# Performance work log

Measured on AMD Instinct MI355X. Metric: run time of the kernel, lower is better.

## Reference

```python
import jax, jax.numpy as jnp
import numpy as np

ALPHA = 0.025
BETA = 0.00025
V_TH = 1.0
EXP_TAU = 50.0          # tau_v / dt
T_NOW = 10.0            # current simulation step counter self.t
REFRAC_STEPS = 2        # refractory_period / dt
INV_TAU_V = float(np.exp(-1.0 / 50.0))   # exp(-dt/tau_v)
INV_TAU_I = float(np.exp(-1.0))          # exp(-dt/tau_i)
INV_TAU_V_PAIR = INV_TAU_V               # tau_v_pair defaults to tau_v
INV_TAU_I_PAIR = INV_TAU_I               # tau_i_pair defaults to tau_i

B, N = 32, 4096


def setup_inputs() -> dict:
    key = jax.random.key(0)
    ks = jax.random.split(key, 8)
    return {
        "inp": jax.random.normal(ks[0], (B, N), jnp.float32),
        "W_rec": jax.random.uniform(ks[1], (N, N), jnp.float32),  # nonneg dense adjacency weights
        "mem_pot": jax.random.normal(ks[2], (B, N), jnp.float32),
        "mem_cur": jax.random.normal(ks[3], (B, N), jnp.float32),
        "mem_pot_paired": jax.random.normal(ks[4], (B, N), jnp.float32),
        "mem_cur_paired": jax.random.normal(ks[5], (B, N), jnp.float32),
        "st": jnp.zeros((N,), jnp.float32),
        "refrac_neurons": jax.random.randint(ks[6], (B, N), 0, 3, jnp.int32),
    }


def reference(inp, W_rec, mem_pot, mem_cur, mem_pot_paired, mem_cur_paired, st, refrac_neurons):
    sign_mask = W_rec > 0  # torch: sign(W_rec) > 0 (weights are nonneg)

    # decrement refractory counters
    refrac = jnp.where(refrac_neurons > 0, refrac_neurons - 1, refrac_neurons)

    # threshold (ceil+clamp -> {0,1} spikes)
    S = jnp.clip(jnp.ceil(mem_pot - V_TH), 0.0, 1.0)                     # (B,N)
    S_paired = jnp.clip(jnp.ceil(mem_pot_paired - V_TH - ALPHA), 0.0, 1.0)

    # ---- plasticity weight update ----
    sp_max = S_paired.max(axis=0)            # (N,)
    st_new = jnp.where(S > 0, T_NOW, st)     # broadcasts (N,) -> (B,N), as in torch
    max_st = st_new.max(axis=0)              # (N,)
    # meshgrid(a,b) with ij indexing: |a-b|[i,j] = |max_st[i]-max_st[j]|
    diff = jnp.abs(max_st[:, None] - max_st[None, :])                    # (N,N)
    update_mask = (sp_max[:, None] > 0) & sign_mask                      # (N,N)
    updated = W_rec + BETA - jnp.where(update_mask,
                                       ALPHA * jnp.exp(diff / EXP_TAU),
                                       0.0)
    updated = jnp.clip(updated, 0.0, 1.0)
    W_new = jnp.where(sign_mask, updated, W_rec)

    # ---- integrate ----
    active = refrac == 0
    mem_cur_n = jnp.where(active, inp + S @ W_new + mem_cur, mem_cur)
    mem_cur_p_n = jnp.where(active, S @ W_new.T + mem_cur_paired, mem_cur_paired)
    mem_pot_n = jnp.where(active, mem_cur_n + mem_pot, mem_pot)
    mem_pot_p_n = jnp.where(active, mem_cur_p_n + mem_pot_paired, mem_pot_paired)

    # leak
    mem_pot_n = mem_pot_n * INV_TAU_V
    mem_cur_n = mem_cur_n * INV_TAU_I
    mem_pot_p_n = mem_pot_p_n * INV_TAU_V_PAIR
    mem_cur_p_n = mem_cur_p_n * INV_TAU_I_PAIR

    # reset spiked neurons
    mem_pot_n = jnp.where(S > 0, 0.0, mem_pot_n)
    mem_pot_p_n = jnp.where(S_paired > 0, 0.0, mem_pot_p_n)
    refrac_new = jnp.where(S > 0, REFRAC_STEPS, refrac)

    return S, mem_pot_n, W_new, mem_cur_n, mem_pot_p_n, mem_cur_p_n, refrac_new
```

## Files before the change

kernel.cpp:

```cpp
#include <hip/hip_runtime.h>
#include <cstdint>
#include <cstddef>

constexpr int N = 4096;
constexpr int B = 32;
constexpr int BN = B * N;
constexpr size_t NN = (size_t)N * N;
constexpr int KCHUNKS = 4;
constexpr int KC = N / KCHUNKS;

constexpr float ALPHA = 0.025f;
constexpr float BETA = 0.00025f;
constexpr float T_NOW = 10.0f;
constexpr float INV_EXP_TAU = 0.02f;
constexpr float INV_TAU_V = 0.98019867f;
constexpr float INV_TAU_I = 0.36787944f;

typedef __attribute__((ext_vector_type(8))) short short8;
typedef __attribute__((ext_vector_type(4))) float f32x4;

__device__ inline unsigned short f2bf(float f) {
  uint32_t u = __float_as_uint(f);
  u += 0x7FFFu + ((u >> 16) & 1u);
  return (unsigned short)(u >> 16);
}

__global__ __launch_bounds__(256) void pass_a(
    const float* __restrict__ mem_pot, const float* __restrict__ mem_pot_p,
    const float* __restrict__ st, float* __restrict__ S_out,
    unsigned short* __restrict__ S_bf,
    uint32_t* __restrict__ maskS, uint32_t* __restrict__ maskSP,
    float* __restrict__ max_st, float* __restrict__ rowfac) {
  int j = blockIdx.x * blockDim.x + threadIdx.x;
  if (j >= N) return;
  float stj = st[j];
  uint32_t ms = 0u, msp = 0u;
  float maxv = -3.0e38f;
  #pragma unroll
  for (int b = 0; b < B; ++b) {
    float p = mem_pot[b * N + j];
    float pp = mem_pot_p[b * N + j];
    bool s = (p - 1.0f) > 0.0f;
    bool sp = ((pp - 1.0f) - ALPHA) > 0.0f;
    S_out[b * N + j] = s ? 1.0f : 0.0f;
    S_bf[b * N + j] = s ? 0x3F80u : 0u;
    ms |= (uint32_t)s << b;
    msp |= (uint32_t)sp << b;
    maxv = fmaxf(maxv, s ? T_NOW : stj);
  }
  maskS[j] = ms;
  maskSP[j] = msp;
  max_st[j] = maxv;
  rowfac[j] = msp ? ALPHA : 0.0f;
}

__global__ __launch_bounds__(256) void pass_b(
    const float* __restrict__ W, const float* __restrict__ max_st,
    const float* __restrict__ rowfac, float* __restrict__ Wout) {
  int i = blockIdx.x;
  int tid = threadIdx.x;
  float mst_i = max_st[i];
  float fac_i = rowfac[i];

  const float4* __restrict__ Wrow = (const float4*)(W + (size_t)i * N);
  float4* __restrict__ Wo = (float4*)(Wout + (size_t)i * N);
  const float4* __restrict__ mstv = (const float4*)max_st;

  float4 w[4], mj[4];
  #pragma unroll
  for (int it = 0; it < 4; ++it) {
    int idx = it * 256 + tid;
    w[it] = Wrow[idx];
    mj[it] = mstv[idx];
  }

  auto upd = [&](float ww, float mstj) -> float {
    float d = fabsf(mst_i - mstj);
    float ex = __expf(d * INV_EXP_TAU);
    float u = ww + BETA - fac_i * ex;
    u = fminf(fmaxf(u, 0.0f), 1.0f);
    return (ww > 0.0f) ? u : ww;
  };

  #pragma unroll
  for (int it = 0; it < 4; ++it) {
    int idx = it * 256 + tid;
    float4 wo;
    wo.x = upd(w[it].x, mj[it].x);
    wo.y = upd(w[it].y, mj[it].y);
    wo.z = upd(w[it].z, mj[it].z);
    wo.w = upd(w[it].w, mj[it].w);
    Wo[idx] = wo;
  }
}

__global__ __launch_bounds__(256) void pass_mfma(
    const float* __restrict__ Wn, const unsigned short* __restrict__ S_bf,
    float* __restrict__ partSW, float* __restrict__ partSWT) {
  int wv = threadIdx.x >> 6;
  int lane = threadIdx.x & 63;
  int ntile = blockIdx.x * 4 + wv;
  int j0 = ntile * 16;
  int kchunk = blockIdx.y;
  int kbase = kchunk * KC;
  int gemm = blockIdx.z;
  int quad = lane >> 4;
  int nl = lane & 15;

  f32x4 acc0 = {0.f, 0.f, 0.f, 0.f};
  f32x4 acc1 = {0.f, 0.f, 0.f, 0.f};
  const unsigned short* A0p = S_bf + (size_t)nl * N;
  const unsigned short* A1p = S_bf + (size_t)(nl + 16) * N;

  if (gemm == 0) {
    #pragma unroll 4
    for (int it = 0; it < KC / 32; ++it) {
      int k0 = kbase + it * 32;
      short8 a0 = *(const short8*)(A0p + k0 + quad * 8);
      short8 a1 = *(const short8*)(A1p + k0 + quad * 8);
      short8 bf;
      #pragma unroll
      for (int i = 0; i < 8; ++i) {
        float f = Wn[(size_t)(k0 + quad * 8 + i) * N + j0 + nl];
        bf[i] = (short)f2bf(f);
      }
      acc0 = __builtin_amdgcn_mfma_f32_16x16x32_bf16(a0, bf, acc0, 0, 0, 0);
      acc1 = __builtin_amdgcn_mfma_f32_16x16x32_bf16(a1, bf, acc1, 0, 0, 0);
    }
  } else {
    const float4* __restrict__ Wr =
        (const float4*)(Wn + (size_t)(j0 + nl) * N);
    #pragma unroll 4
    for (int it = 0; it < KC / 32; ++it) {
      int k0 = kbase + it * 32;
      short8 a0 = *(const short8*)(A0p + k0 + quad * 8);
      short8 a1 = *(const short8*)(A1p + k0 + quad * 8);
      int f4 = (k0 + quad * 8) >> 2;
      float4 f0 = Wr[f4];
      float4 f1 = Wr[f4 + 1];
      short8 bf;
      bf[0] = (short)f2bf(f0.x); bf[1] = (short)f2bf(f0.y);
      bf[2] = (short)f2bf(f0.z); bf[3] = (short)f2bf(f0.w);
      bf[4] = (short)f2bf(f1.x); bf[5] = (short)f2bf(f1.y);
      bf[6] = (short)f2bf(f1.z); bf[7] = (short)f2bf(f1.w);
      acc0 = __builtin_amdgcn_mfma_f32_16x16x32_bf16(a0, bf, acc0, 0, 0, 0);
      acc1 = __builtin_amdgcn_mfma_f32_16x16x32_bf16(a1, bf, acc1, 0, 0, 0);
    }
  }

  float* part = (gemm == 0) ? partSW : partSWT;
  size_t base = (size_t)kchunk * BN + j0 + nl;
  #pragma unroll
  for (int r = 0; r < 4; ++r) {
    part[base + (size_t)(quad * 4 + r) * N] = acc0[r];
    part[base + (size_t)(16 + quad * 4 + r) * N] = acc1[r];
  }
}

__global__ __launch_bounds__(256) void pass_d(
    const float* __restrict__ inp, const float* __restrict__ mem_pot,
    const float* __restrict__ mem_cur, const float* __restrict__ mem_pot_p,
    const float* __restrict__ mem_cur_p, const int* __restrict__ refrac_in,
    const uint32_t* __restrict__ maskS, const uint32_t* __restrict__ maskSP,
    const float* __restrict__ partSW, const float* __restrict__ partSWT,
    float* __restrict__ pot_out, float* __restrict__ cur_out,
    float* __restrict__ potp_out, float* __restrict__ curp_out,
    float* __restrict__ refrac_out) {
  int e = blockIdx.x * 256 + threadIdx.x;
  int b = e >> 12;
  int j = e & (N - 1);

  float SW = 0.0f, SWT = 0.0f;
  #pragma unroll
  for (int c = 0; c < KCHUNKS; ++c) {
    SW += partSW[(size_t)c * BN + e];
    SWT += partSWT[(size_t)c * BN + e];
  }

  int r = refrac_in[e];
  int rd = (r > 0) ? (r - 1) : r;
  bool active = (rd == 0);
  bool s = (maskS[j] >> b) & 1u;
  bool sp = (maskSP[j] >> b) & 1u;
  float cur = mem_cur[e], pot = mem_pot[e];
  float curp = mem_cur_p[e], potp = mem_pot_p[e];

  float cur_n = active ? (inp[e] + SW + cur) : cur;
  float curp_n = active ? (SWT + curp) : curp;
  float pot_n = active ? (cur_n + pot) : pot;
  float potp_n = active ? (curp_n + potp) : potp;

  pot_n *= INV_TAU_V;
  cur_n *= INV_TAU_I;
  potp_n *= INV_TAU_V;
  curp_n *= INV_TAU_I;

  if (s) pot_n = 0.0f;
  if (sp) potp_n = 0.0f;
  int rn = s ? 2 : rd;

  pot_out[e] = pot_n;
  cur_out[e] = cur_n;
  potp_out[e] = potp_n;
  curp_out[e] = curp_n;
  refrac_out[e] = (float)rn;
}

extern "C" void kernel_launch(void* const* d_in, const int* in_sizes, int n_in,
                              void* d_out, int out_size, void* d_ws, size_t ws_size,
                              hipStream_t stream) {
  const float* inp = (const float*)d_in[0];
  const float* W = (const float*)d_in[1];
  const float* mem_pot = (const float*)d_in[2];
  const float* mem_cur = (const float*)d_in[3];
  const float* mem_pot_p = (const float*)d_in[4];
  const float* mem_cur_p = (const float*)d_in[5];
  const float* st = (const float*)d_in[6];
  const int* refrac = (const int*)d_in[7];

  float* out = (float*)d_out;
  float* S_out = out;
  float* pot_out = out + BN;
  float* W_out = out + 2 * (size_t)BN;
  float* cur_out = W_out + NN;
  float* potp_out = cur_out + BN;
  float* curp_out = potp_out + BN;
  float* refrac_out = curp_out + BN;

  uint32_t* maskS = (uint32_t*)d_ws;
  uint32_t* maskSP = maskS + N;
  float* max_st = (float*)(maskSP + N);
  float* rowfac = max_st + N;
  unsigned short* S_bf = (unsigned short*)(rowfac + N);
  float* partSW = (float*)(S_bf + BN);
  float* partSWT = partSW + (size_t)KCHUNKS * BN;

  pass_a<<<N / 256, 256, 0, stream>>>(mem_pot, mem_pot_p, st, S_out, S_bf,
                                      maskS, maskSP, max_st, rowfac);
  pass_b<<<N, 256, 0, stream>>>(W, max_st, rowfac, W_out);
  pass_mfma<<<dim3(64, KCHUNKS, 2), 256, 0, stream>>>(W_out, S_bf, partSW,
                                                      partSWT);
  pass_d<<<BN / 256, 256, 0, stream>>>(inp, mem_pot, mem_cur, mem_pot_p,
                                       mem_cur_p, refrac, maskS, maskSP,
                                       partSW, partSWT, pot_out, cur_out,
                                       potp_out, curp_out, refrac_out);
}
```

Baseline: 167.1 us.

## Fuse weight update into MFMA GEMMs and reduce partials with atomics

Drops the separate weight-update pass. Both GEMM branches now read the original W and apply the plasticity update on the fly. The transposed-GEMM branch also writes the updated W out, so W_new is produced inside the GEMM. This removes one full N×N read and write of the updated matrix. Split-K partial buffers are replaced by float atomicAdd into a single zeroed accumulator (zeroed in pass_a), and KCHUNKS rises to 8. The cost is duplicated exp work in the non-transposed branch and atomic contention, and summation order becomes nondeterministic.

New measurement: 171.2 us. 1.02x slower.

```diff
diff --git a/kernel.cpp b/kernel.cpp
--- a/kernel.cpp
+++ b/kernel.cpp
@@ -6,7 +6,7 @@
 constexpr int B = 32;
 constexpr int BN = B * N;
 constexpr size_t NN = (size_t)N * N;
-constexpr int KCHUNKS = 4;
+constexpr int KCHUNKS = 8;
 constexpr int KC = N / KCHUNKS;
 
 constexpr float ALPHA = 0.025f;
@@ -25,14 +25,27 @@
   return (unsigned short)(u >> 16);
 }
 
+__device__ inline float wupd(float w, float mrow, float frow, float mcol) {
+  float d = fabsf(mrow - mcol);
+  float u = w + BETA - frow * __expf(d * INV_EXP_TAU);
+  u = fminf(fmaxf(u, 0.0f), 1.0f);
+  return (w > 0.0f) ? u : w;
+}
+
 __global__ __launch_bounds__(256) void pass_a(
     const float* __restrict__ mem_pot, const float* __restrict__ mem_pot_p,
     const float* __restrict__ st, float* __restrict__ S_out,
     unsigned short* __restrict__ S_bf,
     uint32_t* __restrict__ maskS, uint32_t* __restrict__ maskSP,
-    float* __restrict__ max_st, float* __restrict__ rowfac) {
+    float* __restrict__ max_st, float* __restrict__ rowfac,
+    float4* __restrict__ zero_region ) {
   int j = blockIdx.x * blockDim.x + threadIdx.x;
   if (j >= N) return;
+
+  float4 z = {0.0f, 0.0f, 0.0f, 0.0f};
+  #pragma unroll
+  for (int k = 0; k < 16; ++k) zero_region[j + k * 4096] = z;
+
   float stj = st[j];
   uint32_t ms = 0u, msp = 0u;
   float maxv = -3.0e38f;
@@ -54,58 +67,28 @@
   rowfac[j] = msp ? ALPHA : 0.0f;
 }
 
-__global__ __launch_bounds__(256) void pass_b(
-    const float* __restrict__ W, const float* __restrict__ max_st,
-    const float* __restrict__ rowfac, float* __restrict__ Wout) {
-  int i = blockIdx.x;
+__global__ __launch_bounds__(256) void pass_fused(
+    const float* __restrict__ W, const unsigned short* __restrict__ S_bf,
+    const float* __restrict__ max_st, const float* __restrict__ rowfac,
+    float* __restrict__ Wout, float* __restrict__ SW, float* __restrict__ SWT) {
+  __shared__ float mstK[KC];
+  __shared__ float facK[KC];
+
   int tid = threadIdx.x;
-  float mst_i = max_st[i];
-  float fac_i = rowfac[i];
-
-  const float4* __restrict__ Wrow = (const float4*)(W + (size_t)i * N);
-  float4* __restrict__ Wo = (float4*)(Wout + (size_t)i * N);
-  const float4* __restrict__ mstv = (const float4*)max_st;
-
-  float4 w[4], mj[4];
-  #pragma unroll
-  for (int it = 0; it < 4; ++it) {
-    int idx = it * 256 + tid;
-    w[it] = Wrow[idx];
-    mj[it] = mstv[idx];
-  }
-
-  auto upd = [&](float ww, float mstj) -> float {
-    float d = fabsf(mst_i - mstj);
-    float ex = __expf(d * INV_EXP_TAU);
-    float u = ww + BETA - fac_i * ex;
-    u = fminf(fmaxf(u, 0.0f), 1.0f);
-    return (ww > 0.0f) ? u : ww;
-  };
-
-  #pragma unroll
-  for (int it = 0; it < 4; ++it) {
-    int idx = it * 256 + tid;
-    float4 wo;
-    wo.x = upd(w[it].x, mj[it].x);
-    wo.y = upd(w[it].y, mj[it].y);
-    wo.z = upd(w[it].z, mj[it].z);
-    wo.w = upd(w[it].w, mj[it].w);
-    Wo[idx] = wo;
-  }
-}
-
-__global__ __launch_bounds__(256) void pass_mfma(
-    const float* __restrict__ Wn, const unsigned short* __restrict__ S_bf,
-    float* __restrict__ partSW, float* __restrict__ partSWT) {
-  int wv = threadIdx.x >> 6;
-  int lane = threadIdx.x & 63;
+  int wv = tid >> 6;
+  int lane = tid & 63;
   int ntile = blockIdx.x * 4 + wv;
   int j0 = ntile * 16;
-  int kchunk = blockIdx.y;
-  int kbase = kchunk * KC;
+  int kbase = blockIdx.y * KC;
   int gemm = blockIdx.z;
   int quad = lane >> 4;
   int nl = lane & 15;
+
+  for (int t = tid; t < KC; t += 256) {
+    mstK[t] = max_st[kbase + t];
+    facK[t] = rowfac[kbase + t];
+  }
+  __syncthreads();
 
   f32x4 acc0 = {0.f, 0.f, 0.f, 0.f};
   f32x4 acc1 = {0.f, 0.f, 0.f, 0.f};
@@ -113,47 +96,74 @@
   const unsigned short* A1p = S_bf + (size_t)(nl + 16) * N;
 
   if (gemm == 0) {
-    #pragma unroll 4
+    float mj = max_st[j0 + nl];
+    #pragma unroll 2
     for (int it = 0; it < KC / 32; ++it) {
-      int k0 = kbase + it * 32;
-      short8 a0 = *(const short8*)(A0p + k0 + quad * 8);
-      short8 a1 = *(const short8*)(A1p + k0 + quad * 8);
+      int ko = it * 32 + quad * 8;
+      int kg = kbase + ko;
+      short8 a0 = *(const short8*)(A0p + kg);
+      short8 a1 = *(const short8*)(A1p + kg);
+      const float* wp = W + (size_t)kg * N + j0 + nl;
+      float4 m4a = *(const float4*)(mstK + ko);
+      float4 m4b = *(const float4*)(mstK + ko + 4);
+      float4 f4a = *(const float4*)(facK + ko);
+      float4 f4b = *(const float4*)(facK + ko + 4);
+      float w[8];
+      #pragma unroll
+      for (int i = 0; i < 8; ++i) w[i] = wp[(size_t)i * N];
       short8 bf;
-      #pragma unroll
-      for (int i = 0; i < 8; ++i) {
-        float f = Wn[(size_t)(k0 + quad * 8 + i) * N + j0 + nl];
-        bf[i] = (short)f2bf(f);
-      }
+      bf[0] = (short)f2bf(wupd(w[0], m4a.x, f4a.x, mj));
+      bf[1] = (short)f2bf(wupd(w[1], m4a.y, f4a.y, mj));
+      bf[2] = (short)f2bf(wupd(w[2], m4a.z, f4a.z, mj));
+      bf[3] = (short)f2bf(wupd(w[3], m4a.w, f4a.w, mj));
+      bf[4] = (short)f2bf(wupd(w[4], m4b.x, f4b.x, mj));
+      bf[5] = (short)f2bf(wupd(w[5], m4b.y, f4b.y, mj));
+      bf[6] = (short)f2bf(wupd(w[6], m4b.z, f4b.z, mj));
+      bf[7] = (short)f2bf(wupd(w[7], m4b.w, f4b.w, mj));
       acc0 = __builtin_amdgcn_mfma_f32_16x16x32_bf16(a0, bf, acc0, 0, 0, 0);
       acc1 = __builtin_amdgcn_mfma_f32_16x16x32_bf16(a1, bf, acc1, 0, 0, 0);
     }
   } else {
-    const float4* __restrict__ Wr =
-        (const float4*)(Wn + (size_t)(j0 + nl) * N);
-    #pragma unroll 4
+    float mi = max_st[j0 + nl];
+    float fi = rowfac[j0 + nl];
+    const float* __restrict__ Wr = W + (size_t)(j0 + nl) * N;
+    float* __restrict__ Wor = Wout + (size_t)(j0 + nl) * N;
+    #pragma unroll 2
     for (int it = 0; it < KC / 32; ++it) {
-      int k0 = kbase + it * 32;
-      short8 a0 = *(const short8*)(A0p + k0 + quad * 8);
-      short8 a1 = *(const short8*)(A1p + k0 + quad * 8);
-      int f4 = (k0 + quad * 8) >> 2;
-      float4 f0 = Wr[f4];
-      float4 f1 = Wr[f4 + 1];
+      int ko = it * 32 + quad * 8;
+      int kg = kbase + ko;
+      short8 a0 = *(const short8*)(A0p + kg);
+      short8 a1 = *(const short8*)(A1p + kg);
+      float4 f0 = *(const float4*)(Wr + kg);
+      float4 f1 = *(const float4*)(Wr + kg + 4);
+      float4 m4a = *(const float4*)(mstK + ko);
+      float4 m4b = *(const float4*)(mstK + ko + 4);
+      float4 u0, u1;
+      u0.x = wupd(f0.x, mi, fi, m4a.x);
+      u0.y = wupd(f0.y, mi, fi, m4a.y);
+      u0.z = wupd(f0.z, mi, fi, m4a.z);
+      u0.w = wupd(f0.w, mi, fi, m4a.w);
+      u1.x = wupd(f1.x, mi, fi, m4b.x);
+      u1.y = wupd(f1.y, mi, fi, m4b.y);
+      u1.z = wupd(f1.z, mi, fi, m4b.z);
+      u1.w = wupd(f1.w, mi, fi, m4b.w);
+      *(float4*)(Wor + kg) = u0;
+      *(float4*)(Wor + kg + 4) = u1;
       short8 bf;
-      bf[0] = (short)f2bf(f0.x); bf[1] = (short)f2bf(f0.y);
-      bf[2] = (short)f2bf(f0.z); bf[3] = (short)f2bf(f0.w);
-      bf[4] = (short)f2bf(f1.x); bf[5] = (short)f2bf(f1.y);
-      bf[6] = (short)f2bf(f1.z); bf[7] = (short)f2bf(f1.w);
+      bf[0] = (short)f2bf(u0.x); bf[1] = (short)f2bf(u0.y);
+      bf[2] = (short)f2bf(u0.z); bf[3] = (short)f2bf(u0.w);
+      bf[4] = (short)f2bf(u1.x); bf[5] = (short)f2bf(u1.y);
+      bf[6] = (short)f2bf(u1.z); bf[7] = (short)f2bf(u1.w);
       acc0 = __builtin_amdgcn_mfma_f32_16x16x32_bf16(a0, bf, acc0, 0, 0, 0);
       acc1 = __builtin_amdgcn_mfma_f32_16x16x32_bf16(a1, bf, acc1, 0, 0, 0);
     }
   }
 
-  float* part = (gemm == 0) ? partSW : partSWT;
-  size_t base = (size_t)kchunk * BN + j0 + nl;
+  float* dst = (gemm == 0) ? SW : SWT;
   #pragma unroll
   for (int r = 0; r < 4; ++r) {
-    part[base + (size_t)(quad * 4 + r) * N] = acc0[r];
-    part[base + (size_t)(16 + quad * 4 + r) * N] = acc1[r];
+    atomicAdd(dst + (size_t)(quad * 4 + r) * N + j0 + nl, acc0[r]);
+    atomicAdd(dst + (size_t)(16 + quad * 4 + r) * N + j0 + nl, acc1[r]);
   }
 }
 
@@ -162,7 +172,7 @@
     const float* __restrict__ mem_cur, const float* __restrict__ mem_pot_p,
     const float* __restrict__ mem_cur_p, const int* __restrict__ refrac_in,
     const uint32_t* __restrict__ maskS, const uint32_t* __restrict__ maskSP,
-    const float* __restrict__ partSW, const float* __restrict__ partSWT,
+    const float* __restrict__ SWbuf, const float* __restrict__ SWTbuf,
     float* __restrict__ pot_out, float* __restrict__ cur_out,
     float* __restrict__ potp_out, float* __restrict__ curp_out,
     float* __restrict__ refrac_out) {
@@ -170,12 +180,8 @@
   int b = e >> 12;
   int j = e & (N - 1);
 
-  float SW = 0.0f, SWT = 0.0f;
-  #pragma unroll
-  for (int c = 0; c < KCHUNKS; ++c) {
-    SW += partSW[(size_t)c * BN + e];
-    SWT += partSWT[(size_t)c * BN + e];
-  }
+  float SW = SWbuf[e];
+  float SWT = SWTbuf[e];
 
   int r = refrac_in[e];
   int rd = (r > 0) ? (r - 1) : r;
@@ -232,16 +238,16 @@
   float* max_st = (float*)(maskSP + N);
   float* rowfac = max_st + N;
   unsigned short* S_bf = (unsigned short*)(rowfac + N);
-  float* partSW = (float*)(S_bf + BN);
-  float* partSWT = partSW + (size_t)KCHUNKS * BN;
+  float* SW = (float*)(S_bf + BN);
+  float* SWT = SW + BN;
 
   pass_a<<<N / 256, 256, 0, stream>>>(mem_pot, mem_pot_p, st, S_out, S_bf,
-                                      maskS, maskSP, max_st, rowfac);
-  pass_b<<<N, 256, 0, stream>>>(W, max_st, rowfac, W_out);
-  pass_mfma<<<dim3(64, KCHUNKS, 2), 256, 0, stream>>>(W_out, S_bf, partSW,
-                                                      partSWT);
+                                      maskS, maskSP, max_st, rowfac,
+                                      (float4*)SW);
+  pass_fused<<<dim3(64, KCHUNKS, 2), 256, 0, stream>>>(W, S_bf, max_st, rowfac,
+                                                       W_out, SW, SWT);
   pass_d<<<BN / 256, 256, 0, stream>>>(inp, mem_pot, mem_cur, mem_pot_p,
                                        mem_cur_p, refrac, maskS, maskSP,
-                                       partSW, partSWT, pot_out, cur_out,
+                                       SW, SWT, pot_out, cur_out,
                                        potp_out, curp_out, refrac_out);
 }
```

## Fuse weight update with both S@W and S@W^T MFMA GEMMs via LDS tiles

Applied to the files above, without the earlier changes.

Merges the elementwise plasticity update and the two bf16 MFMA matmuls into one tiled kernel. Each block updates a 256x128 tile of W, writes W_out, and stages bf16 copies in LDS so that half the waves compute S@W and the other half compute S@W^T from the same tile. This avoids re-reading the 64MB updated W from global memory twice. The cost is many more partial-sum buffers (16 and 32 slices) for the final pass to reduce, plus extra workspace traffic.

Measured after the change: 156.0 us. -6.6%, faster.

```diff
diff --git a/kernel.cpp b/kernel.cpp
--- a/kernel.cpp
+++ b/kernel.cpp
@@ -6,8 +6,13 @@
 constexpr int B = 32;
 constexpr int BN = B * N;
 constexpr size_t NN = (size_t)N * N;
-constexpr int KCHUNKS = 4;
-constexpr int KC = N / KCHUNKS;
+
+constexpr int TI = 256;
+constexpr int TJ = 128;
+constexpr int NIT = N / TI;
+constexpr int NJT = N / TJ;
+constexpr int ISUB = 64;
+constexpr int LDT = TJ + 8;
 
 constexpr float ALPHA = 0.025f;
 constexpr float BETA = 0.00025f;
@@ -23,6 +28,13 @@
   uint32_t u = __float_as_uint(f);
   u += 0x7FFFu + ((u >> 16) & 1u);
   return (unsigned short)(u >> 16);
+}
+
+__device__ inline float wupd(float w, float mrow, float frow, float mcol) {
+  float d = fabsf(mrow - mcol);
+  float u = w + BETA - frow * __expf(d * INV_EXP_TAU);
+  u = fminf(fmaxf(u, 0.0f), 1.0f);
+  return (w > 0.0f) ? u : w;
 }
 
 __global__ __launch_bounds__(256) void pass_a(
@@ -54,106 +66,135 @@
   rowfac[j] = msp ? ALPHA : 0.0f;
 }
 
-__global__ __launch_bounds__(256) void pass_b(
-    const float* __restrict__ W, const float* __restrict__ max_st,
-    const float* __restrict__ rowfac, float* __restrict__ Wout) {
-  int i = blockIdx.x;
+__global__ __launch_bounds__(512, 4) void pass_fused(
+    const float* __restrict__ W, const unsigned short* __restrict__ S_bf,
+    const float* __restrict__ max_st, const float* __restrict__ rowfac,
+    float* __restrict__ Wout, float* __restrict__ partSW,
+    float* __restrict__ partSWT) {
+  __shared__ __align__(16) unsigned short tile[ISUB * LDT];
+  __shared__ float mstI[TI];
+  __shared__ float facI[TI];
+  __shared__ float mstJ[TJ];
+
   int tid = threadIdx.x;
-  float mst_i = max_st[i];
-  float fac_i = rowfac[i];
-
-  const float4* __restrict__ Wrow = (const float4*)(W + (size_t)i * N);
-  float4* __restrict__ Wo = (float4*)(Wout + (size_t)i * N);
-  const float4* __restrict__ mstv = (const float4*)max_st;
-
-  float4 w[4], mj[4];
-  #pragma unroll
-  for (int it = 0; it < 4; ++it) {
-    int idx = it * 256 + tid;
-    w[it] = Wrow[idx];
-    mj[it] = mstv[idx];
-  }
-
-  auto upd = [&](float ww, float mstj) -> float {
-    float d = fabsf(mst_i - mstj);
-    float ex = __expf(d * INV_EXP_TAU);
-    float u = ww + BETA - fac_i * ex;
-    u = fminf(fmaxf(u, 0.0f), 1.0f);
-    return (ww > 0.0f) ? u : ww;
-  };
-
-  #pragma unroll
-  for (int it = 0; it < 4; ++it) {
-    int idx = it * 256 + tid;
-    float4 wo;
-    wo.x = upd(w[it].x, mj[it].x);
-    wo.y = upd(w[it].y, mj[it].y);
-    wo.z = upd(w[it].z, mj[it].z);
-    wo.w = upd(w[it].w, mj[it].w);
-    Wo[idx] = wo;
-  }
-}
-
-__global__ __launch_bounds__(256) void pass_mfma(
-    const float* __restrict__ Wn, const unsigned short* __restrict__ S_bf,
-    float* __restrict__ partSW, float* __restrict__ partSWT) {
-  int wv = threadIdx.x >> 6;
-  int lane = threadIdx.x & 63;
-  int ntile = blockIdx.x * 4 + wv;
-  int j0 = ntile * 16;
-  int kchunk = blockIdx.y;
-  int kbase = kchunk * KC;
-  int gemm = blockIdx.z;
+  int wv = tid >> 6;
+  int lane = tid & 63;
   int quad = lane >> 4;
   int nl = lane & 15;
-
-  f32x4 acc0 = {0.f, 0.f, 0.f, 0.f};
-  f32x4 acc1 = {0.f, 0.f, 0.f, 0.f};
-  const unsigned short* A0p = S_bf + (size_t)nl * N;
-  const unsigned short* A1p = S_bf + (size_t)(nl + 16) * N;
-
-  if (gemm == 0) {
-    #pragma unroll 4
-    for (int it = 0; it < KC / 32; ++it) {
-      int k0 = kbase + it * 32;
-      short8 a0 = *(const short8*)(A0p + k0 + quad * 8);
-      short8 a1 = *(const short8*)(A1p + k0 + quad * 8);
-      short8 bf;
+  int jt = blockIdx.x;
+  int it = blockIdx.y;
+  int i0 = it * TI;
+  int j0 = jt * TJ;
+
+  uint32_t* tileU32 = (uint32_t*)tile;
+
+  if (tid < TI) {
+    mstI[tid] = max_st[i0 + tid];
+    facI[tid] = rowfac[i0 + tid];
+  } else if (tid < TI + TJ) {
+    mstJ[tid - TI] = max_st[j0 + (tid - TI)];
+  }
+
+  float4 pf0, pf1, pf2, pf3;
+  int row = tid >> 5;
+  int c4 = tid & 31;
+  {
+    const float* base = W + (size_t)(i0 + row) * N + j0 + c4 * 4;
+    pf0 = *(const float4*)(base);
+    pf1 = *(const float4*)(base + (size_t)16 * N);
+    pf2 = *(const float4*)(base + (size_t)32 * N);
+    pf3 = *(const float4*)(base + (size_t)48 * N);
+  }
+  __syncthreads();
+
+  f32x4 accA0 = {0.f, 0.f, 0.f, 0.f}, accA1 = {0.f, 0.f, 0.f, 0.f};
+  f32x4 accB0 = {0.f, 0.f, 0.f, 0.f}, accB1 = {0.f, 0.f, 0.f, 0.f};
+
+  for (int isub = 0; isub < TI / ISUB; ++isub) {
+    float4 mj = *(const float4*)(mstJ + c4 * 4);
+    #pragma unroll
+    for (int p = 0; p < 4; ++p) {
+      float4 w4 = (p == 0) ? pf0 : (p == 1) ? pf1 : (p == 2) ? pf2 : pf3;
+      int r = p * 16 + row;
+      int ig = i0 + isub * ISUB + r;
+      float mi = mstI[isub * ISUB + r];
+      float fi = facI[isub * ISUB + r];
+      float4 u;
+      u.x = wupd(w4.x, mi, fi, mj.x);
+      u.y = wupd(w4.y, mi, fi, mj.y);
+      u.z = wupd(w4.z, mi, fi, mj.z);
+      u.w = wupd(w4.w, mi, fi, mj.w);
+      *(float4*)(Wout + (size_t)ig * N + j0 + c4 * 4) = u;
+      uint32_t d0 = (uint32_t)f2bf(u.x) | ((uint32_t)f2bf(u.y) << 16);
+      uint32_t d1 = (uint32_t)f2bf(u.z) | ((uint32_t)f2bf(u.w) << 16);
+      uint2 dd; dd.x = d0; dd.y = d1;
+      *(uint2*)&tileU32[r * (LDT / 2) + c4 * 2] = dd;
+    }
+    if (isub + 1 < TI / ISUB) {
+      const float* base =
+          W + (size_t)(i0 + (isub + 1) * ISUB + row) * N + j0 + c4 * 4;
+      pf0 = *(const float4*)(base);
+      pf1 = *(const float4*)(base + (size_t)16 * N);
+      pf2 = *(const float4*)(base + (size_t)32 * N);
+      pf3 = *(const float4*)(base + (size_t)48 * N);
+    }
+    __syncthreads();
+
+    if (wv < 4) {
+      int js0 = wv * 2, js1 = wv * 2 + 1;
       #pragma unroll
-      for (int i = 0; i < 8; ++i) {
-        float f = Wn[(size_t)(k0 + quad * 8 + i) * N + j0 + nl];
-        bf[i] = (short)f2bf(f);
+      for (int kstep = 0; kstep < 2; ++kstep) {
+        int kl = kstep * 32 + quad * 8;
+        int kglob = i0 + isub * ISUB + kl;
+        short8 a0 = *(const short8*)(S_bf + (size_t)nl * N + kglob);
+        short8 a1 = *(const short8*)(S_bf + (size_t)(nl + 16) * N + kglob);
+        short8 b0, b1;
+        #pragma unroll
+        for (int e = 0; e < 8; ++e) {
+          b0[e] = (short)tile[(kl + e) * LDT + js0 * 16 + nl];
+          b1[e] = (short)tile[(kl + e) * LDT + js1 * 16 + nl];
+        }
+        accA0 = __builtin_amdgcn_mfma_f32_16x16x32_bf16(a0, b0, accA0, 0, 0, 0);
+        accA1 = __builtin_amdgcn_mfma_f32_16x16x32_bf16(a1, b0, accA1, 0, 0, 0);
+        accB0 = __builtin_amdgcn_mfma_f32_16x16x32_bf16(a0, b1, accB0, 0, 0, 0);
+        accB1 = __builtin_amdgcn_mfma_f32_16x16x32_bf16(a1, b1, accB1, 0, 0, 0);
       }
-      acc0 = __builtin_amdgcn_mfma_f32_16x16x32_bf16(a0, bf, acc0, 0, 0, 0);
-      acc1 = __builtin_amdgcn_mfma_f32_16x16x32_bf16(a1, bf, acc1, 0, 0, 0);
-    }
-  } else {
-    const float4* __restrict__ Wr =
-        (const float4*)(Wn + (size_t)(j0 + nl) * N);
-    #pragma unroll 4
-    for (int it = 0; it < KC / 32; ++it) {
-      int k0 = kbase + it * 32;
-      short8 a0 = *(const short8*)(A0p + k0 + quad * 8);
-      short8 a1 = *(const short8*)(A1p + k0 + quad * 8);
-      int f4 = (k0 + quad * 8) >> 2;
-      float4 f0 = Wr[f4];
-      float4 f1 = Wr[f4 + 1];
-      short8 bf;
-      bf[0] = (short)f2bf(f0.x); bf[1] = (short)f2bf(f0.y);
-      bf[2] = (short)f2bf(f0.z); bf[3] = (short)f2bf(f0.w);
-      bf[4] = (short)f2bf(f1.x); bf[5] = (short)f2bf(f1.y);
-      bf[6] = (short)f2bf(f1.z); bf[7] = (short)f2bf(f1.w);
-      acc0 = __builtin_amdgcn_mfma_f32_16x16x32_bf16(a0, bf, acc0, 0, 0, 0);
-      acc1 = __builtin_amdgcn_mfma_f32_16x16x32_bf16(a1, bf, acc1, 0, 0, 0);
-    }
-  }
-
-  float* part = (gemm == 0) ? partSW : partSWT;
-  size_t base = (size_t)kchunk * BN + j0 + nl;
-  #pragma unroll
-  for (int r = 0; r < 4; ++r) {
-    part[base + (size_t)(quad * 4 + r) * N] = acc0[r];
-    part[base + (size_t)(16 + quad * 4 + r) * N] = acc1[r];
+    } else {
+      int ws = wv - 4;
+      int il = ws * 16 + nl;
+      f32x4 g0 = {0.f, 0.f, 0.f, 0.f}, g1 = {0.f, 0.f, 0.f, 0.f};
+      #pragma unroll
+      for (int kstep = 0; kstep < 4; ++kstep) {
+        int kl = kstep * 32 + quad * 8;
+        int kglobJ = j0 + kl;
+        short8 a0 = *(const short8*)(S_bf + (size_t)nl * N + kglobJ);
+        short8 a1 = *(const short8*)(S_bf + (size_t)(nl + 16) * N + kglobJ);
+        short8 bfr = *(const short8*)&tile[il * LDT + kl];
+        g0 = __builtin_amdgcn_mfma_f32_16x16x32_bf16(a0, bfr, g0, 0, 0, 0);
+        g1 = __builtin_amdgcn_mfma_f32_16x16x32_bf16(a1, bfr, g1, 0, 0, 0);
+      }
+      int iglob = i0 + isub * ISUB + il;
+      size_t basew = (size_t)jt * BN + iglob;
+      #pragma unroll
+      for (int r = 0; r < 4; ++r) {
+        partSWT[basew + (size_t)(quad * 4 + r) * N] = g0[r];
+        partSWT[basew + (size_t)(16 + quad * 4 + r) * N] = g1[r];
+      }
+    }
+    if (isub + 1 < TI / ISUB) __syncthreads();
+  }
+
+  if (wv < 4) {
+    int jg0 = j0 + (wv * 2) * 16 + nl;
+    int jg1 = j0 + (wv * 2 + 1) * 16 + nl;
+    size_t baseit = (size_t)it * BN;
+    #pragma unroll
+    for (int r = 0; r < 4; ++r) {
+      partSW[baseit + (size_t)(quad * 4 + r) * N + jg0] = accA0[r];
+      partSW[baseit + (size_t)(16 + quad * 4 + r) * N + jg0] = accA1[r];
+      partSW[baseit + (size_t)(quad * 4 + r) * N + jg1] = accB0[r];
+      partSW[baseit + (size_t)(16 + quad * 4 + r) * N + jg1] = accB1[r];
+    }
   }
 }
 
@@ -172,10 +213,9 @@
 
   float SW = 0.0f, SWT = 0.0f;
   #pragma unroll
-  for (int c = 0; c < KCHUNKS; ++c) {
-    SW += partSW[(size_t)c * BN + e];
-    SWT += partSWT[(size_t)c * BN + e];
-  }
+  for (int c = 0; c < NIT; ++c) SW += partSW[(size_t)c * BN + e];
+  #pragma unroll
+  for (int c = 0; c < NJT; ++c) SWT += partSWT[(size_t)c * BN + e];
 
   int r = refrac_in[e];
   int rd = (r > 0) ? (r - 1) : r;
@@ -233,13 +273,12 @@
   float* rowfac = max_st + N;
   unsigned short* S_bf = (unsigned short*)(rowfac + N);
   float* partSW = (float*)(S_bf + BN);
-  float* partSWT = partSW + (size_t)KCHUNKS * BN;
+  float* partSWT = partSW + (size_t)NIT * BN;
 
   pass_a<<<N / 256, 256, 0, stream>>>(mem_pot, mem_pot_p, st, S_out, S_bf,
                                       maskS, maskSP, max_st, rowfac);
-  pass_b<<<N, 256, 0, stream>>>(W, max_st, rowfac, W_out);
-  pass_mfma<<<dim3(64, KCHUNKS, 2), 256, 0, stream>>>(W_out, S_bf, partSW,
-                                                      partSWT);
+  pass_fused<<<dim3(NJT, NIT), 512, 0, stream>>>(W, S_bf, max_st, rowfac,
+                                                 W_out, partSW, partSWT);
   pass_d<<<BN / 256, 256, 0, stream>>>(inp, mem_pot, mem_cur, mem_pot_p,
                                        mem_cur_p, refrac, maskS, maskSP,
                                        partSW, partSWT, pot_out, cur_out,
```
